# Kernel optimization log

Hardware: AMD Instinct MI355X
Metric: run time of the kernel (lower is better)

## Reference

```python
import jax, jax.numpy as jnp
import numpy as np

B = 16384          # batch size (positions)
NNZ_PER = 32       # active features per position (pieces on board)
F = 768            # 2 colors x 6 pieces x 64 squares
H = 512            # hidden_size


def setup_inputs() -> dict:
    key = jax.random.key(0)
    k1, k2, k3, k4, k5, k6 = jax.random.split(key, 6)
    nnz = B * NNZ_PER
    batch_row = jnp.repeat(jnp.arange(B, dtype=jnp.int64), NNZ_PER)
    stm_feat = jax.random.randint(k1, (nnz,), 0, F, dtype=jnp.int64)
    nstm_feat = jax.random.randint(k2, (nnz,), 0, F, dtype=jnp.int64)
    stm_indices = jnp.stack([batch_row, stm_feat])    # [2, nnz] COO (batch, feature)
    nstm_indices = jnp.stack([batch_row, nstm_feat])  # [2, nnz]
    stm_values = jnp.ones((nnz,), dtype=jnp.float32)   # binary features
    nstm_values = jnp.ones((nnz,), dtype=jnp.float32)
    W_ft = jax.random.normal(k3, (H, F), dtype=jnp.float32) * 0.02
    b_ft = jax.random.normal(k4, (H,), dtype=jnp.float32) * 0.02
    W_out = jax.random.normal(k5, (1, 2 * H), dtype=jnp.float32) * 0.02
    b_out = jax.random.normal(k6, (1,), dtype=jnp.float32) * 0.02
    return {
        "stm_indices": stm_indices,
        "nstm_indices": nstm_indices,
        "stm_values": stm_values,
        "nstm_values": nstm_values,
        "batch_size": B,
        "W_ft": W_ft,
        "b_ft": b_ft,
        "W_out": W_out,
        "b_out": b_out,
    }


def _to_dense(indices, values, batch_size):
    # torch.sparse_coo_tensor(...).to_dense(): duplicates are summed.
    dense = jnp.zeros((batch_size, F), dtype=jnp.float32)
    return dense.at[indices[0], indices[1]].add(values)


def reference(stm_indices, nstm_indices, stm_values, nstm_values, batch_size,
              W_ft, b_ft, W_out, b_out):
    stm_dense = _to_dense(stm_indices, stm_values, batch_size)     # [B, 768]
    nstm_dense = _to_dense(nstm_indices, nstm_values, batch_size)  # [B, 768]
    stm_hidden = stm_dense @ W_ft.T + b_ft     # [B, H]
    nstm_hidden = nstm_dense @ W_ft.T + b_ft   # [B, H]
    hidden = jnp.concatenate([stm_hidden, nstm_hidden], axis=1)  # [B, 2H]
    hidden = jnp.clip(hidden, 0.0, 1.0)
    return jax.nn.sigmoid(hidden @ W_out.T + b_out)  # [B, 1]
```

## Files before the change

kernel.cpp:

```cpp
#include <hip/hip_runtime.h>
#include <hip/hip_fp16.h>

#define B_SZ    16384
#define NNZ_PER 32
#define F_DIM   768
#define H_DIM   512

__global__ __launch_bounds__(256) void transpose_convert(
    const float* __restrict__ W, ushort* __restrict__ Wt)
{
    __shared__ float tile[32][33];
    const int f0 = blockIdx.x * 32;
    const int h0 = blockIdx.y * 32;
    const int tx = threadIdx.x;
    const int ty = threadIdx.y;

#pragma unroll
    for (int i = 0; i < 32; i += 8)
        tile[ty + i][tx] = W[(h0 + ty + i) * F_DIM + f0 + tx];
    __syncthreads();
#pragma unroll
    for (int i = 0; i < 32; i += 8) {
        __half h = __float2half_rn(tile[tx][ty + i]);
        Wt[(f0 + ty + i) * H_DIM + h0 + tx] = *(ushort*)&h;
    }
}

__global__ __launch_bounds__(256, 4) void nnue_fwd(
    const int*   __restrict__ stm_idx,
    const int*   __restrict__ nstm_idx,
    const float* __restrict__ stm_val,
    const float* __restrict__ nstm_val,
    const ushort* __restrict__ Wt,
    const float* __restrict__ b_ft,
    const float* __restrict__ W_out,
    const float* __restrict__ b_out,
    float* __restrict__ out)
{
    const int tid  = threadIdx.x;
    const int w    = tid >> 6;
    const int lane = tid & 63;
    const int b    = blockIdx.x * 4 + w;
    const int NNZ  = B_SZ * NNZ_PER;

    __shared__ unsigned long long sh[4][64];
    {
        const int base = b * NNZ_PER;
        int f; float v;
        if (lane < 32) { f = stm_idx [NNZ + base + lane];        v = stm_val [base + lane]; }
        else           { f = nstm_idx[NNZ + base + (lane - 32)]; v = nstm_val[base + (lane - 32)]; }
        __half2 vv = __float2half2_rn(v);
        unsigned int v2 = *(unsigned int*)&vv;
        sh[w][lane] = ((unsigned long long)v2 << 32) | (unsigned int)f;
    }
    __syncthreads();

    const char* Wb = (const char*)Wt + (lane << 4);

    __half2 z = __float2half2_rn(0.f);
    __half2 s0 = z, s1 = z, s2 = z, s3 = z;
    __half2 n0 = z, n1 = z, n2 = z, n3 = z;

#pragma unroll 8
    for (int j = 0; j < NNZ_PER; ++j) {
        unsigned long long es = sh[w][j];
        unsigned long long en = sh[w][NNZ_PER + j];

        unsigned int fs_ = (unsigned int)es;
        unsigned int v2s = (unsigned int)(es >> 32);
        unsigned int fn_ = (unsigned int)en;
        unsigned int v2n = (unsigned int)(en >> 32);

        uint4 ws = *(const uint4*)(Wb + ((size_t)fs_ << 10));
        uint4 wn = *(const uint4*)(Wb + ((size_t)fn_ << 10));

        __half2 vvs = *(__half2*)&v2s;
        __half2 vvn = *(__half2*)&v2n;

        s0 = __hfma2(*(__half2*)&ws.x, vvs, s0);
        s1 = __hfma2(*(__half2*)&ws.y, vvs, s1);
        s2 = __hfma2(*(__half2*)&ws.z, vvs, s2);
        s3 = __hfma2(*(__half2*)&ws.w, vvs, s3);
        n0 = __hfma2(*(__half2*)&wn.x, vvn, n0);
        n1 = __hfma2(*(__half2*)&wn.y, vvn, n1);
        n2 = __hfma2(*(__half2*)&wn.z, vvn, n2);
        n3 = __hfma2(*(__half2*)&wn.w, vvn, n3);
    }

    const int col = lane * 8;
    float hs[8], hn[8];
    hs[0] = __low2float(s0); hs[1] = __high2float(s0);
    hs[2] = __low2float(s1); hs[3] = __high2float(s1);
    hs[4] = __low2float(s2); hs[5] = __high2float(s2);
    hs[6] = __low2float(s3); hs[7] = __high2float(s3);
    hn[0] = __low2float(n0); hn[1] = __high2float(n0);
    hn[2] = __low2float(n1); hn[3] = __high2float(n1);
    hn[4] = __low2float(n2); hn[5] = __high2float(n2);
    hn[6] = __low2float(n3); hn[7] = __high2float(n3);

    float dot = 0.f;
#pragma unroll
    for (int k = 0; k < 8; ++k) {
        float bf = b_ft[col + k];
        float a = fminf(fmaxf(hs[k] + bf, 0.f), 1.f);
        float c = fminf(fmaxf(hn[k] + bf, 0.f), 1.f);
        dot += a * W_out[col + k] + c * W_out[H_DIM + col + k];
    }

#pragma unroll
    for (int off = 32; off > 0; off >>= 1)
        dot += __shfl_down(dot, off, 64);

    if (lane == 0)
        out[b] = 1.f / (1.f + expf(-(dot + b_out[0])));
}

extern "C" void kernel_launch(void* const* d_in, const int* in_sizes, int n_in,
                              void* d_out, int out_size, void* d_ws, size_t ws_size,
                              hipStream_t stream) {
    const int*   stm_idx  = (const int*)  d_in[0];
    const int*   nstm_idx = (const int*)  d_in[1];
    const float* stm_val  = (const float*)d_in[2];
    const float* nstm_val = (const float*)d_in[3];
    const float* W_ft     = (const float*)d_in[5];
    const float* b_ft     = (const float*)d_in[6];
    const float* W_out    = (const float*)d_in[7];
    const float* b_out    = (const float*)d_in[8];
    float*       out      = (float*)d_out;
    ushort*      Wt       = (ushort*)d_ws;

    dim3 tb(32, 8);
    dim3 tg(F_DIM / 32, H_DIM / 32);
    transpose_convert<<<tg, tb, 0, stream>>>(W_ft, Wt);

    nnue_fwd<<<B_SZ / 4, 256, 0, stream>>>(stm_idx, nstm_idx, stm_val, nstm_val,
                                           Wt, b_ft, W_out, b_out, out);
}
```

Before: 112.9 us.

## Store transposed feature weights as e5m2 bytes and split gathers across half-waves

The transposed weight table is quantized to 8-bit e5m2 (rounded fp16 high byte) instead of fp16, halving gather bytes and the table footprint to 384KB. Each half-wave now handles alternate nonzeros, loading 16 bytes (16 weights) per lane, decoding them to half2 with byte-permute, and accumulating. Partial sums are combined across halves with a shuffle. This trades weight precision (2-bit mantissa) for lower memory traffic and cache footprint, and adds decode ALU work.

```diff
diff --git a/kernel.cpp b/kernel.cpp
--- a/kernel.cpp
+++ b/kernel.cpp
@@ -6,8 +6,20 @@
 #define F_DIM   768
 #define H_DIM   512
 
+typedef unsigned int  uint32;
+typedef unsigned long long uint64;
+typedef unsigned char uchar;
+
+__device__ inline uchar f32_to_e5m2(float x) {
+    __half h = __float2half_rn(x);
+    unsigned short hb = *(unsigned short*)&h;
+    unsigned short lsb = (hb >> 8) & 1;
+    hb = (unsigned short)(hb + 0x7F + lsb);
+    return (uchar)(hb >> 8);
+}
+
 __global__ __launch_bounds__(256) void transpose_convert(
-    const float* __restrict__ W, ushort* __restrict__ Wt)
+    const float* __restrict__ W, uchar* __restrict__ Wt8)
 {
     __shared__ float tile[32][33];
     const int f0 = blockIdx.x * 32;
@@ -20,10 +32,8 @@
         tile[ty + i][tx] = W[(h0 + ty + i) * F_DIM + f0 + tx];
     __syncthreads();
 #pragma unroll
-    for (int i = 0; i < 32; i += 8) {
-        __half h = __float2half_rn(tile[tx][ty + i]);
-        Wt[(f0 + ty + i) * H_DIM + h0 + tx] = *(ushort*)&h;
-    }
+    for (int i = 0; i < 32; i += 8)
+        Wt8[(size_t)(f0 + ty + i) * H_DIM + h0 + tx] = f32_to_e5m2(tile[tx][ty + i]);
 }
 
 __global__ __launch_bounds__(256, 4) void nnue_fwd(
@@ -31,7 +41,7 @@
     const int*   __restrict__ nstm_idx,
     const float* __restrict__ stm_val,
     const float* __restrict__ nstm_val,
-    const ushort* __restrict__ Wt,
+    const uchar* __restrict__ Wt8,
     const float* __restrict__ b_ft,
     const float* __restrict__ W_out,
     const float* __restrict__ b_out,
@@ -40,76 +50,92 @@
     const int tid  = threadIdx.x;
     const int w    = tid >> 6;
     const int lane = tid & 63;
+    const int half = lane >> 5;
+    const int c    = lane & 31;
     const int b    = blockIdx.x * 4 + w;
     const int NNZ  = B_SZ * NNZ_PER;
 
-    __shared__ unsigned long long sh[4][64];
+    __shared__ uint64 sh[4][64];
     {
         const int base = b * NNZ_PER;
         int f; float v;
         if (lane < 32) { f = stm_idx [NNZ + base + lane];        v = stm_val [base + lane]; }
         else           { f = nstm_idx[NNZ + base + (lane - 32)]; v = nstm_val[base + (lane - 32)]; }
         __half2 vv = __float2half2_rn(v);
-        unsigned int v2 = *(unsigned int*)&vv;
-        sh[w][lane] = ((unsigned long long)v2 << 32) | (unsigned int)f;
+        sh[w][lane] = ((uint64)(*(uint32*)&vv) << 32) | (uint32)f;
     }
     __syncthreads();
 
-    const char* Wb = (const char*)Wt + (lane << 4);
+    const uint32 selA = 0x01040004u;
+    const uint32 selB = 0x03040204u;
+    const uint32 coff = (uint32)c << 4;
+    const char*  Wb   = (const char*)Wt8;
 
     __half2 z = __float2half2_rn(0.f);
-    __half2 s0 = z, s1 = z, s2 = z, s3 = z;
-    __half2 n0 = z, n1 = z, n2 = z, n3 = z;
+    __half2 sa[8] = {z,z,z,z,z,z,z,z};
+    __half2 na[8] = {z,z,z,z,z,z,z,z};
+
+#define DECODE_FMA(acc, wv, vv)                                            \
+    {                                                                      \
+        uint32 p;                                                          \
+        p = __builtin_amdgcn_perm(0u, wv.x, selA); acc[0] = __hfma2(*(__half2*)&p, vv, acc[0]); \
+        p = __builtin_amdgcn_perm(0u, wv.x, selB); acc[1] = __hfma2(*(__half2*)&p, vv, acc[1]); \
+        p = __builtin_amdgcn_perm(0u, wv.y, selA); acc[2] = __hfma2(*(__half2*)&p, vv, acc[2]); \
+        p = __builtin_amdgcn_perm(0u, wv.y, selB); acc[3] = __hfma2(*(__half2*)&p, vv, acc[3]); \
+        p = __builtin_amdgcn_perm(0u, wv.z, selA); acc[4] = __hfma2(*(__half2*)&p, vv, acc[4]); \
+        p = __builtin_amdgcn_perm(0u, wv.z, selB); acc[5] = __hfma2(*(__half2*)&p, vv, acc[5]); \
+        p = __builtin_amdgcn_perm(0u, wv.w, selA); acc[6] = __hfma2(*(__half2*)&p, vv, acc[6]); \
+        p = __builtin_amdgcn_perm(0u, wv.w, selB); acc[7] = __hfma2(*(__half2*)&p, vv, acc[7]); \
+    }
 
 #pragma unroll 8
-    for (int j = 0; j < NNZ_PER; ++j) {
-        unsigned long long es = sh[w][j];
-        unsigned long long en = sh[w][NNZ_PER + j];
+    for (int j = 0; j < 16; ++j) {
+        uint64 e = sh[w][2 * j + half];
+        uint32 f = (uint32)e;
+        uint32 v2 = (uint32)(e >> 32);
+        __half2 vv = *(__half2*)&v2;
+        uint4 wv = *(const uint4*)(Wb + (((size_t)f) << 9) + coff);
+        DECODE_FMA(sa, wv, vv);
+    }
+#pragma unroll 8
+    for (int j = 0; j < 16; ++j) {
+        uint64 e = sh[w][32 + 2 * j + half];
+        uint32 f = (uint32)e;
+        uint32 v2 = (uint32)(e >> 32);
+        __half2 vv = *(__half2*)&v2;
+        uint4 wv = *(const uint4*)(Wb + (((size_t)f) << 9) + coff);
+        DECODE_FMA(na, wv, vv);
+    }
+#undef DECODE_FMA
 
-        unsigned int fs_ = (unsigned int)es;
-        unsigned int v2s = (unsigned int)(es >> 32);
-        unsigned int fn_ = (unsigned int)en;
-        unsigned int v2n = (unsigned int)(en >> 32);
-
-        uint4 ws = *(const uint4*)(Wb + ((size_t)fs_ << 10));
-        uint4 wn = *(const uint4*)(Wb + ((size_t)fn_ << 10));
-
-        __half2 vvs = *(__half2*)&v2s;
-        __half2 vvn = *(__half2*)&v2n;
-
-        s0 = __hfma2(*(__half2*)&ws.x, vvs, s0);
-        s1 = __hfma2(*(__half2*)&ws.y, vvs, s1);
-        s2 = __hfma2(*(__half2*)&ws.z, vvs, s2);
-        s3 = __hfma2(*(__half2*)&ws.w, vvs, s3);
-        n0 = __hfma2(*(__half2*)&wn.x, vvn, n0);
-        n1 = __hfma2(*(__half2*)&wn.y, vvn, n1);
-        n2 = __hfma2(*(__half2*)&wn.z, vvn, n2);
-        n3 = __hfma2(*(__half2*)&wn.w, vvn, n3);
+    float s[16], n[16];
+#pragma unroll
+    for (int k = 0; k < 8; ++k) {
+        int mi = *(int*)&sa[k];
+        int oi = __shfl_xor(mi, 32, 64);
+        __half2 o = *(__half2*)&oi;
+        s[2 * k]     = __low2float(sa[k])  + __low2float(o);
+        s[2 * k + 1] = __high2float(sa[k]) + __high2float(o);
+        mi = *(int*)&na[k];
+        oi = __shfl_xor(mi, 32, 64);
+        o  = *(__half2*)&oi;
+        n[2 * k]     = __low2float(na[k])  + __low2float(o);
+        n[2 * k + 1] = __high2float(na[k]) + __high2float(o);
     }
 
-    const int col = lane * 8;
-    float hs[8], hn[8];
-    hs[0] = __low2float(s0); hs[1] = __high2float(s0);
-    hs[2] = __low2float(s1); hs[3] = __high2float(s1);
-    hs[4] = __low2float(s2); hs[5] = __high2float(s2);
-    hs[6] = __low2float(s3); hs[7] = __high2float(s3);
-    hn[0] = __low2float(n0); hn[1] = __high2float(n0);
-    hn[2] = __low2float(n1); hn[3] = __high2float(n1);
-    hn[4] = __low2float(n2); hn[5] = __high2float(n2);
-    hn[6] = __low2float(n3); hn[7] = __high2float(n3);
-
+    const float* bias = b_ft + c * 16;
+    const float* wo   = W_out + half * H_DIM + c * 16;
     float dot = 0.f;
 #pragma unroll
-    for (int k = 0; k < 8; ++k) {
-        float bf = b_ft[col + k];
-        float a = fminf(fmaxf(hs[k] + bf, 0.f), 1.f);
-        float c = fminf(fmaxf(hn[k] + bf, 0.f), 1.f);
-        dot += a * W_out[col + k] + c * W_out[H_DIM + col + k];
+    for (int k = 0; k < 16; ++k) {
+        float hv = half ? n[k] : s[k];
+        float a  = fminf(fmaxf(hv + bias[k], 0.f), 1.f);
+        dot += a * wo[k];
     }
 
 #pragma unroll
     for (int off = 32; off > 0; off >>= 1)
-        dot += __shfl_down(dot, off, 64);
+        dot += __shfl_xor(dot, off, 64);
 
     if (lane == 0)
         out[b] = 1.f / (1.f + expf(-(dot + b_out[0])));
@@ -127,12 +153,12 @@
     const float* W_out    = (const float*)d_in[7];
     const float* b_out    = (const float*)d_in[8];
     float*       out      = (float*)d_out;
-    ushort*      Wt       = (ushort*)d_ws;
+    uchar*       Wt8      = (uchar*)d_ws;
 
     dim3 tb(32, 8);
     dim3 tg(F_DIM / 32, H_DIM / 32);
-    transpose_convert<<<tg, tb, 0, stream>>>(W_ft, Wt);
+    transpose_convert<<<tg, tb, 0, stream>>>(W_ft, Wt8);
 
     nnue_fwd<<<B_SZ / 4, 256, 0, stream>>>(stm_idx, nstm_idx, stm_val, nstm_val,
-                                           Wt, b_ft, W_out, b_out, out);
+                                           Wt8, b_ft, W_out, b_out, out);
 }
```

After: 105.4 us. -6.7%, faster.
